# Kernel tuning notes

Hardware: AMD Instinct MI355X
Metric: run time of the kernel (lower is better)

## Reference

```python
import jax, jax.numpy as jnp
import numpy as np

N, IN_DIM, HID, LAT, E = 8192, 512, 256, 128, 262144


def gcn_conv(x, W, b, src, dst, n):
    # PyG-style GCNConv: linear transform, add self-loops, D^-1/2 A D^-1/2 aggregation, bias.
    h = x @ W                                                  # [n, out]
    loops = jnp.arange(n)
    s = jnp.concatenate([src, loops])
    d = jnp.concatenate([dst, loops])
    deg = jax.ops.segment_sum(jnp.ones(s.shape[0], x.dtype), d, num_segments=n)
    dinv = jnp.where(deg > 0, jax.lax.rsqrt(deg), jnp.zeros((), x.dtype))
    norm = dinv[s] * dinv[d]                                   # [E+n]
    out = jax.ops.segment_sum(h[s] * norm[:, None], d, num_segments=n)
    return out + b


def setup_inputs() -> dict:
    key = jax.random.key(0)
    ks = jax.random.split(key, 9)
    x = jax.random.normal(ks[0], (N, IN_DIM), dtype=jnp.float32)
    edge_index = jax.random.randint(ks[1], (2, E), 0, N, dtype=jnp.int64)
    eps = jax.random.normal(ks[2], (N, LAT), dtype=jnp.float32)
    # Glorot-ish scaled params
    W1 = jax.random.normal(ks[3], (IN_DIM, HID), dtype=jnp.float32) / np.sqrt(IN_DIM)
    b1 = jnp.zeros((HID,), jnp.float32)
    Wmu = jax.random.normal(ks[4], (HID, LAT), dtype=jnp.float32) / np.sqrt(HID)
    bmu = jnp.zeros((LAT,), jnp.float32)
    Wls = jax.random.normal(ks[5], (HID, LAT), dtype=jnp.float32) / np.sqrt(HID)
    bls = jnp.zeros((LAT,), jnp.float32)
    return {"x": x, "edge_index": edge_index, "eps": eps,
            "W1": W1, "b1": b1, "Wmu": Wmu, "bmu": bmu, "Wls": Wls, "bls": bls}


def reference(x, edge_index, eps, W1, b1, Wmu, bmu, Wls, bls):
    src, dst = edge_index[0], edge_index[1]
    n = x.shape[0]
    h = jax.nn.relu(gcn_conv(x, W1, b1, src, dst, n))          # [N, HID]
    mu = gcn_conv(h, Wmu, bmu, src, dst, n)                    # [N, LAT]
    logstd = gcn_conv(h, Wls, bls, src, dst, n)                # [N, LAT]
    z = eps * jnp.exp(logstd) + mu                             # reparametrize (training mode)
    adj_recon = jax.nn.sigmoid(z @ z.T)                        # [N, N]
    return adj_recon, mu, logstd
```

## Files before the change

kernel.cpp:

```cpp
#include <hip/hip_runtime.h>

#define N_NODES 8192
#define IN_DIM  512
#define HID     256
#define LAT     128
#define NEDGE   262144

typedef __attribute__((ext_vector_type(8))) short  bf16x8;
typedef __attribute__((ext_vector_type(4))) float  f32x4;
typedef unsigned short u16;

static __device__ inline u16 f2bf(float f) {
    unsigned u = __float_as_uint(f);
    unsigned r = (u + 0x7fffu + ((u >> 16) & 1u)) >> 16;
    return (u16)r;
}
static __device__ inline float bf2f(u16 s) {
    return __uint_as_float(((unsigned)s) << 16);
}


__global__ __launch_bounds__(256) void count_kernel(const int* __restrict__ dst,
                                                    int* __restrict__ cnt) {
    int e = blockIdx.x * 256 + threadIdx.x;
    atomicAdd(&cnt[dst[e]], 1);
}

__global__ __launch_bounds__(256) void dinv_kernel(const int* __restrict__ cnt,
                                                   float* __restrict__ dinv) {
    int v = blockIdx.x * 256 + threadIdx.x;
    dinv[v] = rsqrtf((float)cnt[v] + 1.0f);
}

__global__ __launch_bounds__(256) void scan_kernel(const int* __restrict__ cnt,
                                                   int* __restrict__ rowptr,
                                                   int* __restrict__ cursor) {
    __shared__ int part[256];
    const int t = threadIdx.x;
    const int base = t * 32;
    int local[32];
    int s = 0;
#pragma unroll
    for (int i = 0; i < 32; ++i) { local[i] = s; s += cnt[base + i]; }
    part[t] = s;
    __syncthreads();
    for (int off = 1; off < 256; off <<= 1) {
        int v = 0;
        if (t >= off) v = part[t - off];
        __syncthreads();
        if (t >= off) part[t] += v;
        __syncthreads();
    }
    int pre = (t == 0) ? 0 : part[t - 1];
#pragma unroll
    for (int i = 0; i < 32; ++i) {
        int r = pre + local[i];
        rowptr[base + i] = r;
        cursor[base + i] = r;
    }
    if (t == 255) rowptr[8192] = part[255];
}

__global__ __launch_bounds__(256) void fill_kernel(const int* __restrict__ src,
                                                   const int* __restrict__ dst,
                                                   int* __restrict__ cursor,
                                                   int* __restrict__ ebuf) {
    int e = blockIdx.x * 256 + threadIdx.x;
    int pos = atomicAdd(&cursor[dst[e]], 1);
    ebuf[pos] = src[e];
}

__global__ __launch_bounds__(256) void gemm_f32(const float* __restrict__ A,
                                                const float* __restrict__ B,
                                                float* __restrict__ C,
                                                int Ktot, int ldb, int ldc, int coff) {
    __shared__ float As[16][68];
    __shared__ float Bs[16][64];
    const int tid = threadIdx.x;
    const int tx = tid & 15, ty = tid >> 4;
    const int rowBase = blockIdx.y * 64, colBase = blockIdx.x * 64;

    float acc[4][4] = {};
    const int am = rowBase + (tid >> 2);
    const int ak = (tid & 3) * 4;
    const int bk = tid >> 4;
    const int bn = colBase + (tid & 15) * 4;

    for (int k0 = 0; k0 < Ktot; k0 += 16) {
        f32x4 av = *(const f32x4*)(A + (size_t)am * Ktot + k0 + ak);
        f32x4 bv = *(const f32x4*)(B + (size_t)(k0 + bk) * ldb + bn);
#pragma unroll
        for (int j = 0; j < 4; ++j) As[ak + j][tid >> 2] = av[j];
        *(f32x4*)&Bs[bk][(tid & 15) * 4] = bv;
        __syncthreads();
#pragma unroll
        for (int kk = 0; kk < 16; ++kk) {
            f32x4 a = *(const f32x4*)&As[kk][ty * 4];
            f32x4 b = *(const f32x4*)&Bs[kk][tx * 4];
#pragma unroll
            for (int i = 0; i < 4; ++i)
#pragma unroll
                for (int j = 0; j < 4; ++j)
                    acc[i][j] += a[i] * b[j];
        }
        __syncthreads();
    }
#pragma unroll
    for (int i = 0; i < 4; ++i) {
        int r = rowBase + ty * 4 + i;
        f32x4 v = { acc[i][0], acc[i][1], acc[i][2], acc[i][3] };
        *(f32x4*)(C + (size_t)r * ldc + coff + colBase + tx * 4) = v;
    }
}

__global__ __launch_bounds__(256) void gather1_kernel(const float* __restrict__ pre1,
                                                      float* __restrict__ h1,
                                                      const int* __restrict__ rowptr,
                                                      const int* __restrict__ ebuf,
                                                      const float* __restrict__ dinv,
                                                      const float* __restrict__ b1) {
    const int wave = threadIdx.x >> 6, lane = threadIdx.x & 63;
    const int v = blockIdx.x * 4 + wave;
    const int c = lane * 4;
    const float dv = dinv[v];
    f32x4 acc = *(const f32x4*)(pre1 + (size_t)v * HID + c);
    acc *= dv * dv;
    int i = rowptr[v], end = rowptr[v + 1];
    for (; i + 1 < end; i += 2) {
        int s0 = ebuf[i], s1 = ebuf[i + 1];
        float n0 = dv * dinv[s0], n1 = dv * dinv[s1];
        f32x4 h0 = *(const f32x4*)(pre1 + (size_t)s0 * HID + c);
        f32x4 h1v = *(const f32x4*)(pre1 + (size_t)s1 * HID + c);
#pragma unroll
        for (int j = 0; j < 4; ++j) acc[j] += n0 * h0[j] + n1 * h1v[j];
    }
    if (i < end) {
        int s0 = ebuf[i];
        float n0 = dv * dinv[s0];
        f32x4 h0 = *(const f32x4*)(pre1 + (size_t)s0 * HID + c);
#pragma unroll
        for (int j = 0; j < 4; ++j) acc[j] += n0 * h0[j];
    }
    f32x4 bb = *(const f32x4*)(b1 + c);
#pragma unroll
    for (int j = 0; j < 4; ++j) acc[j] = fmaxf(acc[j] + bb[j], 0.0f);
    *(f32x4*)(h1 + (size_t)v * HID + c) = acc;
}

__global__ __launch_bounds__(256) void gather2_kernel(const float* __restrict__ pre2,
                                                      const int* __restrict__ rowptr,
                                                      const int* __restrict__ ebuf,
                                                      const float* __restrict__ dinv,
                                                      const float* __restrict__ bmu,
                                                      const float* __restrict__ bls,
                                                      const float* __restrict__ eps,
                                                      float* __restrict__ out_mu,
                                                      float* __restrict__ out_ls,
                                                      u16* __restrict__ zhi,
                                                      u16* __restrict__ zlo) {
    const int wave = threadIdx.x >> 6, lane = threadIdx.x & 63;
    const int v = blockIdx.x * 4 + wave;
    const int c = lane * 4;
    const float dv = dinv[v];
    f32x4 acc = *(const f32x4*)(pre2 + (size_t)v * HID + c);
    acc *= dv * dv;
    int i = rowptr[v], end = rowptr[v + 1];
    for (; i + 1 < end; i += 2) {
        int s0 = ebuf[i], s1 = ebuf[i + 1];
        float n0 = dv * dinv[s0], n1 = dv * dinv[s1];
        f32x4 h0 = *(const f32x4*)(pre2 + (size_t)s0 * HID + c);
        f32x4 h1v = *(const f32x4*)(pre2 + (size_t)s1 * HID + c);
#pragma unroll
        for (int j = 0; j < 4; ++j) acc[j] += n0 * h0[j] + n1 * h1v[j];
    }
    if (i < end) {
        int s0 = ebuf[i];
        float n0 = dv * dinv[s0];
        f32x4 h0 = *(const f32x4*)(pre2 + (size_t)s0 * HID + c);
#pragma unroll
        for (int j = 0; j < 4; ++j) acc[j] += n0 * h0[j];
    }
    const float* bias = (lane < 32) ? (bmu + c) : (bls + (c - 128));
    f32x4 bb = *(const f32x4*)bias;
#pragma unroll
    for (int j = 0; j < 4; ++j) acc[j] += bb[j];

    f32x4 other;
#pragma unroll
    for (int j = 0; j < 4; ++j) other[j] = __shfl(acc[j], (lane + 32) & 63, 64);

    if (lane < 32) {
        int idx = v * LAT + c;
        f32x4 ep = *(const f32x4*)(eps + idx);
        *(f32x4*)(out_mu + idx) = acc;
#pragma unroll
        for (int j = 0; j < 4; ++j) {
            float z = ep[j] * __expf(other[j]) + acc[j];
            u16 hi = f2bf(z);
            zhi[idx + j] = hi;
            zlo[idx + j] = f2bf(z - bf2f(hi));
        }
    } else {
        int idx = v * LAT + (c - 128);
        *(f32x4*)(out_ls + idx) = acc;
    }
}

__global__ __launch_bounds__(256) void zzt_kernel(const u16* __restrict__ zhi,
                                                  const u16* __restrict__ zlo,
                                                  float* __restrict__ out) {
    const int lane = threadIdx.x & 63;
    const int wave = threadIdx.x >> 6;
    const int l16 = lane & 15, quad = lane >> 4;
    const int rowBase = blockIdx.y * 128 + (wave >> 1) * 64;
    const int colBase = blockIdx.x * 128 + (wave & 1) * 64;

    f32x4 acc[4][4] = {};

#pragma unroll
    for (int k0 = 0; k0 < LAT; k0 += 32) {
        const int kk = k0 + quad * 8;
        bf16x8 ah[4], al[4], bh[4], bl[4];
#pragma unroll
        for (int r = 0; r < 4; ++r) {
            int row = rowBase + r * 16 + l16;
            ah[r] = *(const bf16x8*)(zhi + (size_t)row * LAT + kk);
            al[r] = *(const bf16x8*)(zlo + (size_t)row * LAT + kk);
        }
#pragma unroll
        for (int c = 0; c < 4; ++c) {
            int row = colBase + c * 16 + l16;
            bh[c] = *(const bf16x8*)(zhi + (size_t)row * LAT + kk);
            bl[c] = *(const bf16x8*)(zlo + (size_t)row * LAT + kk);
        }
#pragma unroll
        for (int r = 0; r < 4; ++r)
#pragma unroll
            for (int c = 0; c < 4; ++c) {
                acc[r][c] = __builtin_amdgcn_mfma_f32_16x16x32_bf16(ah[r], bh[c], acc[r][c], 0, 0, 0);
                acc[r][c] = __builtin_amdgcn_mfma_f32_16x16x32_bf16(ah[r], bl[c], acc[r][c], 0, 0, 0);
                acc[r][c] = __builtin_amdgcn_mfma_f32_16x16x32_bf16(al[r], bh[c], acc[r][c], 0, 0, 0);
            }
    }

#pragma unroll
    for (int r = 0; r < 4; ++r)
#pragma unroll
        for (int c = 0; c < 4; ++c)
#pragma unroll
            for (int i = 0; i < 4; ++i) {
                int orow = rowBase + r * 16 + quad * 4 + i;
                int ocol = colBase + c * 16 + l16;
                float t = acc[r][c][i];
                out[(size_t)orow * N_NODES + ocol] = 1.0f / (1.0f + __expf(-t));
            }
}

extern "C" void kernel_launch(void* const* d_in, const int* in_sizes, int n_in,
                              void* d_out, int out_size, void* d_ws, size_t ws_size,
                              hipStream_t stream) {
    const float* x   = (const float*)d_in[0];
    const int*   ei  = (const int*)d_in[1];
    const float* eps = (const float*)d_in[2];
    const float* W1  = (const float*)d_in[3];
    const float* b1  = (const float*)d_in[4];
    const float* Wmu = (const float*)d_in[5];
    const float* bmu = (const float*)d_in[6];
    const float* Wls = (const float*)d_in[7];
    const float* bls = (const float*)d_in[8];
    const int* src = ei;
    const int* dst = ei + NEDGE;

    float* out = (float*)d_out;
    float* pre1 = out;
    float* h1   = out + 2097152;
    float* pre2 = out + 4194304;
    int*   ibase  = (int*)(out + 6291456);
    int*   cnt    = ibase;
    int*   rowptr = ibase + 8192;
    int*   cursor = ibase + 16385;
    int*   ebuf   = ibase + 24577;
    float* out_mu = out + 67108864;
    float* out_ls = out + 68157440;

    float* dinv = (float*)d_ws;
    u16* zhi = (u16*)((char*)d_ws + 32768);
    u16* zlo = (u16*)((char*)d_ws + 32768 + 2097152);

    hipMemsetAsync(cnt, 0, 8192 * sizeof(int), stream);

    count_kernel<<<NEDGE / 256, 256, 0, stream>>>(dst, cnt);
    dinv_kernel<<<N_NODES / 256, 256, 0, stream>>>(cnt, dinv);
    scan_kernel<<<1, 256, 0, stream>>>(cnt, rowptr, cursor);
    fill_kernel<<<NEDGE / 256, 256, 0, stream>>>(src, dst, cursor, ebuf);

    gemm_f32<<<dim3(256 / 64, N_NODES / 64), 256, 0, stream>>>(x, W1, pre1, 512, 256, 256, 0);
    gather1_kernel<<<N_NODES / 4, 256, 0, stream>>>(pre1, h1, rowptr, ebuf, dinv, b1);

    gemm_f32<<<dim3(2, N_NODES / 64), 256, 0, stream>>>(h1, Wmu, pre2, 256, 128, 256, 0);
    gemm_f32<<<dim3(2, N_NODES / 64), 256, 0, stream>>>(h1, Wls, pre2, 256, 128, 256, 128);

    gather2_kernel<<<N_NODES / 4, 256, 0, stream>>>(pre2, rowptr, ebuf, dinv, bmu, bls, eps,
                                                    out_mu, out_ls, zhi, zlo);

    zzt_kernel<<<dim3(64, 64), 256, 0, stream>>>(zhi, zlo, out);
}
```

Before: 544.5 us.

## Replace fp32 SIMT GEMMs with split-bf16 MFMA GEMMs and fuse mu/logstd projections

Converts x, the weights, and h1 into hi/lo bf16 pairs and computes the dense projections with 16x16x32 bf16 MFMA, using three products to approximate fp32 accuracy. The two latent-layer GEMMs are merged into one launch over concatenated transposed weights, and gather1 writes its ReLU output directly in split-bf16 form. The aim is to move the GEMM cost from FP32 vector ALUs onto matrix cores. In exchange it adds conversion kernels and extra memory traffic, and the new GEMM reads operands from global memory without LDS staging.

```diff
diff --git a/kernel.cpp b/kernel.cpp
--- a/kernel.cpp
+++ b/kernel.cpp
@@ -9,6 +9,7 @@
 typedef __attribute__((ext_vector_type(8))) short  bf16x8;
 typedef __attribute__((ext_vector_type(4))) float  f32x4;
 typedef unsigned short u16;
+typedef __attribute__((ext_vector_type(4))) unsigned short u16x4;
 
 static __device__ inline u16 f2bf(float f) {
     unsigned u = __float_as_uint(f);
@@ -70,51 +71,91 @@
     ebuf[pos] = src[e];
 }
 
-__global__ __launch_bounds__(256) void gemm_f32(const float* __restrict__ A,
-                                                const float* __restrict__ B,
-                                                float* __restrict__ C,
-                                                int Ktot, int ldb, int ldc, int coff) {
-    __shared__ float As[16][68];
-    __shared__ float Bs[16][64];
-    const int tid = threadIdx.x;
-    const int tx = tid & 15, ty = tid >> 4;
-    const int rowBase = blockIdx.y * 64, colBase = blockIdx.x * 64;
-
-    float acc[4][4] = {};
-    const int am = rowBase + (tid >> 2);
-    const int ak = (tid & 3) * 4;
-    const int bk = tid >> 4;
-    const int bn = colBase + (tid & 15) * 4;
-
-    for (int k0 = 0; k0 < Ktot; k0 += 16) {
-        f32x4 av = *(const f32x4*)(A + (size_t)am * Ktot + k0 + ak);
-        f32x4 bv = *(const f32x4*)(B + (size_t)(k0 + bk) * ldb + bn);
-#pragma unroll
-        for (int j = 0; j < 4; ++j) As[ak + j][tid >> 2] = av[j];
-        *(f32x4*)&Bs[bk][(tid & 15) * 4] = bv;
-        __syncthreads();
-#pragma unroll
-        for (int kk = 0; kk < 16; ++kk) {
-            f32x4 a = *(const f32x4*)&As[kk][ty * 4];
-            f32x4 b = *(const f32x4*)&Bs[kk][tx * 4];
-#pragma unroll
-            for (int i = 0; i < 4; ++i)
-#pragma unroll
-                for (int j = 0; j < 4; ++j)
-                    acc[i][j] += a[i] * b[j];
-        }
-        __syncthreads();
-    }
-#pragma unroll
-    for (int i = 0; i < 4; ++i) {
-        int r = rowBase + ty * 4 + i;
-        f32x4 v = { acc[i][0], acc[i][1], acc[i][2], acc[i][3] };
-        *(f32x4*)(C + (size_t)r * ldc + coff + colBase + tx * 4) = v;
-    }
+
+__global__ __launch_bounds__(256) void convx_kernel(const float* __restrict__ X,
+                                                    u16* __restrict__ xh,
+                                                    u16* __restrict__ xl) {
+    int t = blockIdx.x * 256 + threadIdx.x;
+    f32x4 v = *(const f32x4*)(X + (size_t)t * 4);
+    u16x4 h, l;
+#pragma unroll
+    for (int j = 0; j < 4; ++j) {
+        h[j] = f2bf(v[j]);
+        l[j] = f2bf(v[j] - bf2f(h[j]));
+    }
+    *(u16x4*)(xh + (size_t)t * 4) = h;
+    *(u16x4*)(xl + (size_t)t * 4) = l;
+}
+
+__global__ __launch_bounds__(256) void convw_kernel(const float* __restrict__ W,
+                                                    u16* __restrict__ th,
+                                                    u16* __restrict__ tl,
+                                                    int K, int N, int Kld, int roff) {
+    int e = blockIdx.x * 256 + threadIdx.x;
+    if (e >= K * N) return;
+    int k = e / N, n = e - k * N;
+    float f = W[e];
+    u16 hi = f2bf(f);
+    u16 lo = f2bf(f - bf2f(hi));
+    size_t o = (size_t)(roff + n) * Kld + k;
+    th[o] = hi;
+    tl[o] = lo;
+}
+
+__global__ __launch_bounds__(256) void gemm_mfma(const u16* __restrict__ Ah,
+                                                 const u16* __restrict__ Al,
+                                                 const u16* __restrict__ Bth,
+                                                 const u16* __restrict__ Btl,
+                                                 float* __restrict__ C,
+                                                 int K, int ldc) {
+    const int lane = threadIdx.x & 63;
+    const int wave = threadIdx.x >> 6;
+    const int l16 = lane & 15, quad = lane >> 4;
+    const int rowBase = blockIdx.y * 128 + (wave >> 1) * 64;
+    const int colBase = blockIdx.x * 128 + (wave & 1) * 64;
+
+    f32x4 acc[4][4] = {};
+
+    for (int k0 = 0; k0 < K; k0 += 32) {
+        const int kk = k0 + quad * 8;
+        bf16x8 ah[4], al[4], bh[4], bl[4];
+#pragma unroll
+        for (int r = 0; r < 4; ++r) {
+            int row = rowBase + r * 16 + l16;
+            ah[r] = *(const bf16x8*)(Ah + (size_t)row * K + kk);
+            al[r] = *(const bf16x8*)(Al + (size_t)row * K + kk);
+        }
+#pragma unroll
+        for (int c = 0; c < 4; ++c) {
+            int row = colBase + c * 16 + l16;
+            bh[c] = *(const bf16x8*)(Bth + (size_t)row * K + kk);
+            bl[c] = *(const bf16x8*)(Btl + (size_t)row * K + kk);
+        }
+#pragma unroll
+        for (int r = 0; r < 4; ++r)
+#pragma unroll
+            for (int c = 0; c < 4; ++c) {
+                acc[r][c] = __builtin_amdgcn_mfma_f32_16x16x32_bf16(ah[r], bh[c], acc[r][c], 0, 0, 0);
+                acc[r][c] = __builtin_amdgcn_mfma_f32_16x16x32_bf16(ah[r], bl[c], acc[r][c], 0, 0, 0);
+                acc[r][c] = __builtin_amdgcn_mfma_f32_16x16x32_bf16(al[r], bh[c], acc[r][c], 0, 0, 0);
+            }
+    }
+
+#pragma unroll
+    for (int r = 0; r < 4; ++r)
+#pragma unroll
+        for (int c = 0; c < 4; ++c)
+#pragma unroll
+            for (int i = 0; i < 4; ++i) {
+                int orow = rowBase + r * 16 + quad * 4 + i;
+                int ocol = colBase + c * 16 + l16;
+                C[(size_t)orow * ldc + ocol] = acc[r][c][i];
+            }
 }
 
 __global__ __launch_bounds__(256) void gather1_kernel(const float* __restrict__ pre1,
-                                                      float* __restrict__ h1,
+                                                      u16* __restrict__ h1h,
+                                                      u16* __restrict__ h1l,
                                                       const int* __restrict__ rowptr,
                                                       const int* __restrict__ ebuf,
                                                       const float* __restrict__ dinv,
@@ -142,9 +183,15 @@
         for (int j = 0; j < 4; ++j) acc[j] += n0 * h0[j];
     }
     f32x4 bb = *(const f32x4*)(b1 + c);
-#pragma unroll
-    for (int j = 0; j < 4; ++j) acc[j] = fmaxf(acc[j] + bb[j], 0.0f);
-    *(f32x4*)(h1 + (size_t)v * HID + c) = acc;
+    u16x4 hv, lv;
+#pragma unroll
+    for (int j = 0; j < 4; ++j) {
+        float h = fmaxf(acc[j] + bb[j], 0.0f);
+        hv[j] = f2bf(h);
+        lv[j] = f2bf(h - bf2f(hv[j]));
+    }
+    *(u16x4*)(h1h + (size_t)v * HID + c) = hv;
+    *(u16x4*)(h1l + (size_t)v * HID + c) = lv;
 }
 
 __global__ __launch_bounds__(256) void gather2_kernel(const float* __restrict__ pre2,
@@ -273,13 +320,20 @@
 
     float* out = (float*)d_out;
     float* pre1 = out;
-    float* h1   = out + 2097152;
-    float* pre2 = out + 4194304;
-    int*   ibase  = (int*)(out + 6291456);
+    float* pre2 = out + 2097152;
+    int*   ibase  = (int*)(out + 4194304);
     int*   cnt    = ibase;
     int*   rowptr = ibase + 8192;
     int*   cursor = ibase + 16385;
     int*   ebuf   = ibase + 24577;
+    u16* xhi    = (u16*)(out + 4587520);
+    u16* xlo    = (u16*)(out + 6684672);
+    u16* h1hi   = (u16*)(out + 8781824);
+    u16* h1lo   = (u16*)(out + 9830400);
+    u16* w1thi  = (u16*)(out + 10878976);
+    u16* w1tlo  = (u16*)(out + 11010048);
+    u16* wcathi = (u16*)(out + 11141120);
+    u16* wcatlo = (u16*)(out + 11173888);
     float* out_mu = out + 67108864;
     float* out_ls = out + 68157440;
 
@@ -294,11 +348,17 @@
     scan_kernel<<<1, 256, 0, stream>>>(cnt, rowptr, cursor);
     fill_kernel<<<NEDGE / 256, 256, 0, stream>>>(src, dst, cursor, ebuf);
 
-    gemm_f32<<<dim3(256 / 64, N_NODES / 64), 256, 0, stream>>>(x, W1, pre1, 512, 256, 256, 0);
-    gather1_kernel<<<N_NODES / 4, 256, 0, stream>>>(pre1, h1, rowptr, ebuf, dinv, b1);
-
-    gemm_f32<<<dim3(2, N_NODES / 64), 256, 0, stream>>>(h1, Wmu, pre2, 256, 128, 256, 0);
-    gemm_f32<<<dim3(2, N_NODES / 64), 256, 0, stream>>>(h1, Wls, pre2, 256, 128, 256, 128);
+    convx_kernel<<<4096, 256, 0, stream>>>(x, xhi, xlo);
+    convw_kernel<<<(IN_DIM * HID) / 256, 256, 0, stream>>>(W1, w1thi, w1tlo, IN_DIM, HID, IN_DIM, 0);
+    convw_kernel<<<(HID * LAT) / 256, 256, 0, stream>>>(Wmu, wcathi, wcatlo, HID, LAT, HID, 0);
+    convw_kernel<<<(HID * LAT) / 256, 256, 0, stream>>>(Wls, wcathi, wcatlo, HID, LAT, HID, LAT);
+
+    gemm_mfma<<<dim3(HID / 128, N_NODES / 128), 256, 0, stream>>>(xhi, xlo, w1thi, w1tlo,
+                                                                  pre1, IN_DIM, HID);
+    gather1_kernel<<<N_NODES / 4, 256, 0, stream>>>(pre1, h1hi, h1lo, rowptr, ebuf, dinv, b1);
+
+    gemm_mfma<<<dim3(HID / 128, N_NODES / 128), 256, 0, stream>>>(h1hi, h1lo, wcathi, wcatlo,
+                                                                  pre2, HID, HID);
 
     gather2_kernel<<<N_NODES / 4, 256, 0, stream>>>(pre2, rowptr, ebuf, dinv, bmu, bls, eps,
                                                     out_mu, out_ls, zhi, zlo);
```

Result: no change. 544.8 us (+0.1%).
